# Performance work log

Hardware: AMD Instinct MI355X
Metric: run time of the kernel (lower is better)

Reference implementation:

```python
import jax, jax.numpy as jnp
import numpy as np

MAX_LENGTH = 256
WIDTH = 4


def _attention_matrix(a, b):
    # a, b: (B, M, D) with M = max_length + width - 1
    # euclidean match score: 1 / (1 + ||a_i - b_j||_2)
    sq = (
        jnp.sum(a * a, axis=-1)[:, :, None]
        + jnp.sum(b * b, axis=-1)[:, None, :]
        - 2.0 * jnp.einsum('bid,bjd->bij', a, b)
    )
    dist = jnp.sqrt(jnp.maximum(sq, 0.0))
    return 1.0 / (1.0 + dist)  # (B, M, M)


def reference(x1, x2):
    # x1, x2: (B, 1, M, D), M = MAX_LENGTH + WIDTH - 1
    a = x1[:, 0]  # (B, M, D)
    b = x2[:, 0]
    A = _attention_matrix(a, b)  # (B, M, M), A[b,i,j] = score(a_i, b_j)
    # row_sum over dim i of A[:,:,k] weights x1 column k; col analogously for x2.
    w_a = jnp.sum(A, axis=1)  # (B, M): sum_i A[i, k]
    w_b = jnp.sum(A, axis=2)  # (B, M): sum_j A[k, j]
    y1 = w_a[:, :, None] * a  # (B, M, D)
    y2 = w_b[:, :, None] * b
    # sliding-window sum of width WIDTH: w[j] = sum_{k=j}^{j+WIDTH-1} y[k]
    w1 = sum(y1[:, d:d + MAX_LENGTH, :] for d in range(WIDTH))
    w2 = sum(y2[:, d:d + MAX_LENGTH, :] for d in range(WIDTH))
    return (w1[:, None], w2[:, None])  # (B, 1, MAX_LENGTH, D) each


def setup_inputs() -> dict:
    key = jax.random.key(0)
    k1, k2 = jax.random.split(key)
    B, M, D = 128, MAX_LENGTH + WIDTH - 1, 512
    x1 = jax.random.normal(k1, (B, 1, M, D), dtype=jnp.float32)
    x2 = jax.random.normal(k2, (B, 1, M, D), dtype=jnp.float32)
    return {"x1": x1, "x2": x2}
```

## Files before the change

### kernel.cpp

```cpp
#include <hip/hip_runtime.h>

#define BATCH 128
#define M 259
#define D 512
#define T 256
#define NM (BATCH * M)
#define OUTHALF (BATCH * T * D)

typedef __bf16 bf16;
typedef __bf16 bf16x4 __attribute__((ext_vector_type(4)));
typedef __bf16 bf16x8 __attribute__((ext_vector_type(8)));
typedef float f32x4 __attribute__((ext_vector_type(4)));


__global__ void k_norms(const float* __restrict__ x1, const float* __restrict__ x2,
                        float* __restrict__ ws) {
    int wave = blockIdx.x * 4 + (threadIdx.x >> 6);
    int lane = threadIdx.x & 63;
    if (wave >= NM) return;
    const float4* p1 = (const float4*)(x1 + (size_t)wave * D);
    const float4* p2 = (const float4*)(x2 + (size_t)wave * D);
    float s1 = 0.f, s2 = 0.f;
#pragma unroll
    for (int q = 0; q < 2; ++q) {
        float4 v = p1[lane + q * 64];
        s1 += v.x * v.x + v.y * v.y + v.z * v.z + v.w * v.w;
        float4 w = p2[lane + q * 64];
        s2 += w.x * w.x + w.y * w.y + w.z * w.z + w.w * w.w;
    }
#pragma unroll
    for (int off = 32; off > 0; off >>= 1) {
        s1 += __shfl_xor(s1, off);
        s2 += __shfl_xor(s2, off);
    }
    if (lane == 0) {
        ws[wave]          = s1;
        ws[NM + wave]     = s2;
        ws[2 * NM + wave] = 0.f;
        ws[3 * NM + wave] = 0.f;
    }
}

#define BT 96
#define BK 64
#define NTL 3

__launch_bounds__(256)
__global__ void k_pairs(const float* __restrict__ x1, const float* __restrict__ x2,
                        float* __restrict__ ws) {
    __shared__ __align__(16) bf16 As[BT * BK];
    __shared__ __align__(16) bf16 Bs[BT * BK];

    int s   = blockIdx.x;
    int bid = (s & 7) * 144 + (s >> 3);
    int b   = bid / 9;
    int ti  = (bid % 9) / 3;
    int tj  = bid % 3;
    int i0  = ti * BT, j0 = tj * BT;

    int t    = threadIdx.x;
    int lane = t & 63;
    int w    = t >> 6;
    int wm   = w >> 1, wn = w & 1;
    int iw   = i0 + wm * 48;
    int jw   = j0 + wn * 48;

    const float* Ab = x1 + (size_t)b * M * D;
    const float* Bb = x2 + (size_t)b * M * D;

    const float* pa[6];
    const float* pb[6];
    int c4 = (t & 15) * 4;
#pragma unroll
    for (int p = 0; p < 6; ++p) {
        int ra = min(i0 + p * 16 + (t >> 4), M - 1);
        int rb = min(j0 + p * 16 + (t >> 4), M - 1);
        pa[p] = Ab + (size_t)ra * D + c4;
        pb[p] = Bb + (size_t)rb * D + c4;
    }
    int wslot   = (t & 15) >> 1;
    int wwithin = (t & 1) * 4;
    int wr_off[6];
#pragma unroll
    for (int p = 0; p < 6; ++p) {
        int row = p * 16 + (t >> 4);
        wr_off[p] = row * BK + ((wslot ^ (row & 7)) << 3) + wwithin;
    }

    int a_off[3][2], b_off[3][2];
#pragma unroll
    for (int fm = 0; fm < 3; ++fm) {
        int rowa = wm * 48 + fm * 16 + (lane & 15);
        int rowb = wn * 48 + fm * 16 + (lane & 15);
#pragma unroll
        for (int kk = 0; kk < 2; ++kk) {
            int slot = kk * 4 + (lane >> 4);
            a_off[fm][kk] = rowa * BK + ((slot ^ (rowa & 7)) << 3);
            b_off[fm][kk] = rowb * BK + ((slot ^ (rowb & 7)) << 3);
        }
    }

    f32x4 acc[3][3];
#pragma unroll
    for (int fm = 0; fm < 3; ++fm)
#pragma unroll
        for (int fn = 0; fn < 3; ++fn) acc[fm][fn] = (f32x4)0.f;

    for (int k0 = 0; k0 < D; k0 += BK) {
        float4 va[6], vb[6];
#pragma unroll
        for (int p = 0; p < 6; ++p) {
            va[p] = *(const float4*)(pa[p] + k0);
            vb[p] = *(const float4*)(pb[p] + k0);
        }
        __syncthreads();
#pragma unroll
        for (int p = 0; p < 6; ++p) {
            bf16x4 ca = { (bf16)va[p].x, (bf16)va[p].y, (bf16)va[p].z, (bf16)va[p].w };
            bf16x4 cb = { (bf16)vb[p].x, (bf16)vb[p].y, (bf16)vb[p].z, (bf16)vb[p].w };
            *(bf16x4*)&As[wr_off[p]] = ca;
            *(bf16x4*)&Bs[wr_off[p]] = cb;
        }
        __syncthreads();
#pragma unroll
        for (int kk = 0; kk < 2; ++kk) {
            bf16x8 af[3], bfr[3];
#pragma unroll
            for (int fm = 0; fm < 3; ++fm) af[fm]  = *(const bf16x8*)&As[a_off[fm][kk]];
#pragma unroll
            for (int fn = 0; fn < 3; ++fn) bfr[fn] = *(const bf16x8*)&Bs[b_off[fn][kk]];
#pragma unroll
            for (int fm = 0; fm < 3; ++fm)
#pragma unroll
                for (int fn = 0; fn < 3; ++fn)
                    acc[fm][fn] = __builtin_amdgcn_mfma_f32_16x16x32_bf16(
                        af[fm], bfr[fn], acc[fm][fn], 0, 0, 0);
        }
    }

    int b_off_w = b * M;
    float na_[3][4], nb_[3];
#pragma unroll
    for (int fm = 0; fm < 3; ++fm)
#pragma unroll
        for (int r = 0; r < 4; ++r) {
            int i = iw + fm * 16 + (lane >> 4) * 4 + r;
            na_[fm][r] = (i < M) ? ws[b_off_w + i] : 0.f;
        }
#pragma unroll
    for (int fn = 0; fn < 3; ++fn) {
        int j = jw + fn * 16 + (lane & 15);
        nb_[fn] = (j < M) ? ws[NM + b_off_w + j] : 0.f;
    }

    float rs[3][4];
    float cs[3];
#pragma unroll
    for (int fm = 0; fm < 3; ++fm)
#pragma unroll
        for (int r = 0; r < 4; ++r) rs[fm][r] = 0.f;
#pragma unroll
    for (int fn = 0; fn < 3; ++fn) cs[fn] = 0.f;

#pragma unroll
    for (int fm = 0; fm < 3; ++fm) {
#pragma unroll
        for (int fn = 0; fn < 3; ++fn) {
#pragma unroll
            for (int r = 0; r < 4; ++r) {
                int i = iw + fm * 16 + (lane >> 4) * 4 + r;
                int j = jw + fn * 16 + (lane & 15);
                float av = 0.f;
                if (i < M && j < M) {
                    float sq   = na_[fm][r] + nb_[fn] - 2.f * acc[fm][fn][r];
                    float dist = sqrtf(fmaxf(sq, 0.f));
                    av = 1.f / (1.f + dist);
                }
                rs[fm][r] += av;
                cs[fn]    += av;
            }
        }
    }

#pragma unroll
    for (int fm = 0; fm < 3; ++fm)
#pragma unroll
        for (int r = 0; r < 4; ++r) {
            float v = rs[fm][r];
            v += __shfl_xor(v, 1); v += __shfl_xor(v, 2);
            v += __shfl_xor(v, 4); v += __shfl_xor(v, 8);
            int i = iw + fm * 16 + (lane >> 4) * 4 + r;
            if ((lane & 15) == 0 && i < M) atomicAdd(&ws[3 * NM + b_off_w + i], v);
        }
#pragma unroll
    for (int fn = 0; fn < 3; ++fn) {
        float v = cs[fn];
        v += __shfl_xor(v, 16); v += __shfl_xor(v, 32);
        int j = jw + fn * 16 + (lane & 15);
        if ((lane >> 4) == 0 && j < M) atomicAdd(&ws[2 * NM + b_off_w + j], v);
    }
}

__global__ void k_out(const float* __restrict__ x1, const float* __restrict__ x2,
                      const float* __restrict__ ws, float* __restrict__ out) {
    int bid   = blockIdx.x;
    int which = bid & 1;
    int dh    = (bid >> 1) & 1;
    int tc    = (bid >> 2) & 3;
    int b     = bid >> 4;
    int d     = dh * 256 + threadIdx.x;
    const float* src  = which ? x2 : x1;
    const float* w    = ws + (which ? 3 * NM : 2 * NM) + b * M;
    const float* rows = src + (size_t)b * M * D + d;
    float* o = out + (size_t)which * OUTHALF + ((size_t)b * T + tc * 64) * D + d;
    int t0 = tc * 64;
    float v0 = rows[(size_t)(t0 + 0) * D];
    float v1 = rows[(size_t)(t0 + 1) * D];
    float v2 = rows[(size_t)(t0 + 2) * D];
    float s0 = w[t0 + 0], s1 = w[t0 + 1], s2 = w[t0 + 2];
    for (int tt = 0; tt < 64; ++tt) {
        int tg = t0 + tt;
        float v3 = rows[(size_t)(tg + 3) * D];
        float s3 = w[tg + 3];
        o[(size_t)tt * D] = s0 * v0 + s1 * v1 + s2 * v2 + s3 * v3;
        v0 = v1; v1 = v2; v2 = v3;
        s0 = s1; s1 = s2; s2 = s3;
    }
}

extern "C" void kernel_launch(void* const* d_in, const int* in_sizes, int n_in,
                              void* d_out, int out_size, void* d_ws, size_t ws_size,
                              hipStream_t stream) {
    const float* x1 = (const float*)d_in[0];
    const float* x2 = (const float*)d_in[1];
    float* out = (float*)d_out;
    float* ws  = (float*)d_ws;

    k_norms<<<NM / 4, 256, 0, stream>>>(x1, x2, ws);
    k_pairs<<<BATCH * NTL * NTL, 256, 0, stream>>>(x1, x2, ws);
    k_out<<<BATCH * 16, 256, 0, stream>>>(x1, x2, ws, out);
}
```

Baseline: 112.6 us.

## Fuse row norms into pair GEMM, prefetch next K tile, vectorize output kernel

Drops the separate norm kernel: squared norms are now accumulated from the fp32 tiles already loaded in the pairwise GEMM and shared through LDS, which removes a full extra read of both inputs. A small zeroing kernel replaces it for the atomic accumulators. The GEMM loop also software-prefetches the next K slice into registers before the MMA work. The output kernel switches to float4 loads and stores with 32-row chunks and 128 threads. Costs are higher register pressure in k_pairs, and each tile now recomputes the norms of rows it shares with other tiles.

New measurement: 125.3 us. 11.3% more time.

```diff
diff --git a/kernel.cpp b/kernel.cpp
--- a/kernel.cpp
+++ b/kernel.cpp
@@ -13,32 +13,9 @@
 typedef float f32x4 __attribute__((ext_vector_type(4)));
 
 
-__global__ void k_norms(const float* __restrict__ x1, const float* __restrict__ x2,
-                        float* __restrict__ ws) {
-    int wave = blockIdx.x * 4 + (threadIdx.x >> 6);
-    int lane = threadIdx.x & 63;
-    if (wave >= NM) return;
-    const float4* p1 = (const float4*)(x1 + (size_t)wave * D);
-    const float4* p2 = (const float4*)(x2 + (size_t)wave * D);
-    float s1 = 0.f, s2 = 0.f;
-#pragma unroll
-    for (int q = 0; q < 2; ++q) {
-        float4 v = p1[lane + q * 64];
-        s1 += v.x * v.x + v.y * v.y + v.z * v.z + v.w * v.w;
-        float4 w = p2[lane + q * 64];
-        s2 += w.x * w.x + w.y * w.y + w.z * w.z + w.w * w.w;
-    }
-#pragma unroll
-    for (int off = 32; off > 0; off >>= 1) {
-        s1 += __shfl_xor(s1, off);
-        s2 += __shfl_xor(s2, off);
-    }
-    if (lane == 0) {
-        ws[wave]          = s1;
-        ws[NM + wave]     = s2;
-        ws[2 * NM + wave] = 0.f;
-        ws[3 * NM + wave] = 0.f;
-    }
+__global__ void k_zero(float4* __restrict__ ws4) {
+    int i = blockIdx.x * 256 + threadIdx.x;
+    if (i < (2 * NM + 3) / 4) ws4[i] = make_float4(0.f, 0.f, 0.f, 0.f);
 }
 
 #define BT 96
@@ -50,6 +27,8 @@
                         float* __restrict__ ws) {
     __shared__ __align__(16) bf16 As[BT * BK];
     __shared__ __align__(16) bf16 Bs[BT * BK];
+    __shared__ float na_s[BT];
+    __shared__ float nb_s[BT];
 
     int s   = blockIdx.x;
     int bid = (s & 7) * 144 + (s >> 3);
@@ -106,20 +85,40 @@
 #pragma unroll
         for (int fn = 0; fn < 3; ++fn) acc[fm][fn] = (f32x4)0.f;
 
+    float sa[6], sb[6];
+#pragma unroll
+    for (int p = 0; p < 6; ++p) { sa[p] = 0.f; sb[p] = 0.f; }
+
+    float4 va[6], vb[6];
+#pragma unroll
+    for (int p = 0; p < 6; ++p) {
+        va[p] = *(const float4*)(pa[p]);
+        vb[p] = *(const float4*)(pb[p]);
+    }
+
     for (int k0 = 0; k0 < D; k0 += BK) {
-        float4 va[6], vb[6];
+        bf16x4 ca[6], cb[6];
 #pragma unroll
         for (int p = 0; p < 6; ++p) {
-            va[p] = *(const float4*)(pa[p] + k0);
-            vb[p] = *(const float4*)(pb[p] + k0);
+            sa[p] += va[p].x * va[p].x + va[p].y * va[p].y
+                   + va[p].z * va[p].z + va[p].w * va[p].w;
+            sb[p] += vb[p].x * vb[p].x + vb[p].y * vb[p].y
+                   + vb[p].z * vb[p].z + vb[p].w * vb[p].w;
+            ca[p] = { (bf16)va[p].x, (bf16)va[p].y, (bf16)va[p].z, (bf16)va[p].w };
+            cb[p] = { (bf16)vb[p].x, (bf16)vb[p].y, (bf16)vb[p].z, (bf16)vb[p].w };
         }
         __syncthreads();
 #pragma unroll
         for (int p = 0; p < 6; ++p) {
-            bf16x4 ca = { (bf16)va[p].x, (bf16)va[p].y, (bf16)va[p].z, (bf16)va[p].w };
-            bf16x4 cb = { (bf16)vb[p].x, (bf16)vb[p].y, (bf16)vb[p].z, (bf16)vb[p].w };
-            *(bf16x4*)&As[wr_off[p]] = ca;
-            *(bf16x4*)&Bs[wr_off[p]] = cb;
+            *(bf16x4*)&As[wr_off[p]] = ca[p];
+            *(bf16x4*)&Bs[wr_off[p]] = cb[p];
+        }
+        if (k0 + BK < D) {
+#pragma unroll
+            for (int p = 0; p < 6; ++p) {
+                va[p] = *(const float4*)(pa[p] + k0 + BK);
+                vb[p] = *(const float4*)(pb[p] + k0 + BK);
+            }
         }
         __syncthreads();
 #pragma unroll
@@ -138,20 +137,30 @@
         }
     }
 
+#pragma unroll
+    for (int p = 0; p < 6; ++p) {
+        float v1 = sa[p], v2 = sb[p];
+        v1 += __shfl_xor(v1, 1); v1 += __shfl_xor(v1, 2);
+        v1 += __shfl_xor(v1, 4); v1 += __shfl_xor(v1, 8);
+        v2 += __shfl_xor(v2, 1); v2 += __shfl_xor(v2, 2);
+        v2 += __shfl_xor(v2, 4); v2 += __shfl_xor(v2, 8);
+        if ((t & 15) == 0) {
+            na_s[p * 16 + (t >> 4)] = v1;
+            nb_s[p * 16 + (t >> 4)] = v2;
+        }
+    }
+    __syncthreads();
+
     int b_off_w = b * M;
     float na_[3][4], nb_[3];
 #pragma unroll
     for (int fm = 0; fm < 3; ++fm)
 #pragma unroll
-        for (int r = 0; r < 4; ++r) {
-            int i = iw + fm * 16 + (lane >> 4) * 4 + r;
-            na_[fm][r] = (i < M) ? ws[b_off_w + i] : 0.f;
-        }
-#pragma unroll
-    for (int fn = 0; fn < 3; ++fn) {
-        int j = jw + fn * 16 + (lane & 15);
-        nb_[fn] = (j < M) ? ws[NM + b_off_w + j] : 0.f;
-    }
+        for (int r = 0; r < 4; ++r)
+            na_[fm][r] = na_s[wm * 48 + fm * 16 + (lane >> 4) * 4 + r];
+#pragma unroll
+    for (int fn = 0; fn < 3; ++fn)
+        nb_[fn] = nb_s[wn * 48 + fn * 16 + (lane & 15)];
 
     float rs[3][4];
     float cs[3];
@@ -190,14 +199,14 @@
             v += __shfl_xor(v, 1); v += __shfl_xor(v, 2);
             v += __shfl_xor(v, 4); v += __shfl_xor(v, 8);
             int i = iw + fm * 16 + (lane >> 4) * 4 + r;
-            if ((lane & 15) == 0 && i < M) atomicAdd(&ws[3 * NM + b_off_w + i], v);
+            if ((lane & 15) == 0 && i < M) atomicAdd(&ws[NM + b_off_w + i], v);
         }
 #pragma unroll
     for (int fn = 0; fn < 3; ++fn) {
         float v = cs[fn];
         v += __shfl_xor(v, 16); v += __shfl_xor(v, 32);
         int j = jw + fn * 16 + (lane & 15);
-        if ((lane >> 4) == 0 && j < M) atomicAdd(&ws[2 * NM + b_off_w + j], v);
+        if ((lane >> 4) == 0 && j < M) atomicAdd(&ws[b_off_w + j], v);
     }
 }
 
@@ -205,24 +214,28 @@
                       const float* __restrict__ ws, float* __restrict__ out) {
     int bid   = blockIdx.x;
     int which = bid & 1;
-    int dh    = (bid >> 1) & 1;
-    int tc    = (bid >> 2) & 3;
+    int tc    = (bid >> 1) & 7;
     int b     = bid >> 4;
-    int d     = dh * 256 + threadIdx.x;
+    int d4    = threadIdx.x << 2;
     const float* src  = which ? x2 : x1;
-    const float* w    = ws + (which ? 3 * NM : 2 * NM) + b * M;
-    const float* rows = src + (size_t)b * M * D + d;
-    float* o = out + (size_t)which * OUTHALF + ((size_t)b * T + tc * 64) * D + d;
-    int t0 = tc * 64;
-    float v0 = rows[(size_t)(t0 + 0) * D];
-    float v1 = rows[(size_t)(t0 + 1) * D];
-    float v2 = rows[(size_t)(t0 + 2) * D];
-    float s0 = w[t0 + 0], s1 = w[t0 + 1], s2 = w[t0 + 2];
-    for (int tt = 0; tt < 64; ++tt) {
-        int tg = t0 + tt;
-        float v3 = rows[(size_t)(tg + 3) * D];
-        float s3 = w[tg + 3];
-        o[(size_t)tt * D] = s0 * v0 + s1 * v1 + s2 * v2 + s3 * v3;
+    const float* wgt  = ws + (which ? NM : 0) + b * M;
+    const float* rows = src + (size_t)b * M * D + d4;
+    float* o = out + (size_t)which * OUTHALF + ((size_t)b * T + tc * 32) * D + d4;
+    int t0 = tc * 32;
+    float4 v0 = *(const float4*)(rows + (size_t)(t0 + 0) * D);
+    float4 v1 = *(const float4*)(rows + (size_t)(t0 + 1) * D);
+    float4 v2 = *(const float4*)(rows + (size_t)(t0 + 2) * D);
+    float s0 = wgt[t0 + 0], s1 = wgt[t0 + 1], s2 = wgt[t0 + 2];
+#pragma unroll 4
+    for (int tt = 0; tt < 32; ++tt) {
+        float4 v3 = *(const float4*)(rows + (size_t)(t0 + tt + 3) * D);
+        float s3  = wgt[t0 + tt + 3];
+        float4 r;
+        r.x = s0 * v0.x + s1 * v1.x + s2 * v2.x + s3 * v3.x;
+        r.y = s0 * v0.y + s1 * v1.y + s2 * v2.y + s3 * v3.y;
+        r.z = s0 * v0.z + s1 * v1.z + s2 * v2.z + s3 * v3.z;
+        r.w = s0 * v0.w + s1 * v1.w + s2 * v2.w + s3 * v3.w;
+        *(float4*)(o + (size_t)tt * D) = r;
         v0 = v1; v1 = v2; v2 = v3;
         s0 = s1; s1 = s2; s2 = s3;
     }
@@ -236,7 +249,7 @@
     float* out = (float*)d_out;
     float* ws  = (float*)d_ws;
 
-    k_norms<<<NM / 4, 256, 0, stream>>>(x1, x2, ws);
+    k_zero<<<(2 * NM / 4 + 255) / 256, 256, 0, stream>>>((float4*)ws);
     k_pairs<<<BATCH * NTL * NTL, 256, 0, stream>>>(x1, x2, ws);
-    k_out<<<BATCH * 16, 256, 0, stream>>>(x1, x2, ws, out);
-}
+    k_out<<<BATCH * 16, 128, 0, stream>>>(x1, x2, ws, out);
+}
```

## Double-buffer LDS tiles in pair GEMM and vectorize sliding-window output kernel

Applied to the files above, without the earlier changes.

The pair kernel now uses two LDS buffers, so the bf16 conversion and store of the next K tile and the global prefetch of the tile after it are issued after the MFMAs on the current tile. This cuts the two barriers per K step down to one and hides global load latency behind compute, at the cost of doubled LDS use (about 49KB per block), which could lower occupancy. The output kernel switches to float4 loads and stores with 128 threads, each block covering 32 rows, to cut the instruction count of this memory-bound pass.

Result: slower. 117.3 us (+4.2%).

```diff
diff --git a/kernel.cpp b/kernel.cpp
--- a/kernel.cpp
+++ b/kernel.cpp
@@ -48,8 +48,8 @@
 __launch_bounds__(256)
 __global__ void k_pairs(const float* __restrict__ x1, const float* __restrict__ x2,
                         float* __restrict__ ws) {
-    __shared__ __align__(16) bf16 As[BT * BK];
-    __shared__ __align__(16) bf16 Bs[BT * BK];
+    __shared__ __align__(16) bf16 As[2][BT * BK];
+    __shared__ __align__(16) bf16 Bs[2][BT * BK];
 
     int s   = blockIdx.x;
     int bid = (s & 7) * 144 + (s >> 3);
@@ -106,35 +106,58 @@
 #pragma unroll
         for (int fn = 0; fn < 3; ++fn) acc[fm][fn] = (f32x4)0.f;
 
+    float4 va[6], vb[6];
+#pragma unroll
+    for (int p = 0; p < 6; ++p) {
+        va[p] = *(const float4*)(pa[p]);
+        vb[p] = *(const float4*)(pb[p]);
+    }
+#pragma unroll
+    for (int p = 0; p < 6; ++p) {
+        bf16x4 ca = { (bf16)va[p].x, (bf16)va[p].y, (bf16)va[p].z, (bf16)va[p].w };
+        bf16x4 cb = { (bf16)vb[p].x, (bf16)vb[p].y, (bf16)vb[p].z, (bf16)vb[p].w };
+        *(bf16x4*)&As[0][wr_off[p]] = ca;
+        *(bf16x4*)&Bs[0][wr_off[p]] = cb;
+    }
+    __syncthreads();
+#pragma unroll
+    for (int p = 0; p < 6; ++p) {
+        va[p] = *(const float4*)(pa[p] + BK);
+        vb[p] = *(const float4*)(pb[p] + BK);
+    }
+
     for (int k0 = 0; k0 < D; k0 += BK) {
-        float4 va[6], vb[6];
-#pragma unroll
-        for (int p = 0; p < 6; ++p) {
-            va[p] = *(const float4*)(pa[p] + k0);
-            vb[p] = *(const float4*)(pb[p] + k0);
-        }
-        __syncthreads();
-#pragma unroll
-        for (int p = 0; p < 6; ++p) {
-            bf16x4 ca = { (bf16)va[p].x, (bf16)va[p].y, (bf16)va[p].z, (bf16)va[p].w };
-            bf16x4 cb = { (bf16)vb[p].x, (bf16)vb[p].y, (bf16)vb[p].z, (bf16)vb[p].w };
-            *(bf16x4*)&As[wr_off[p]] = ca;
-            *(bf16x4*)&Bs[wr_off[p]] = cb;
-        }
-        __syncthreads();
+        int cur = (k0 >> 6) & 1;
 #pragma unroll
         for (int kk = 0; kk < 2; ++kk) {
             bf16x8 af[3], bfr[3];
 #pragma unroll
-            for (int fm = 0; fm < 3; ++fm) af[fm]  = *(const bf16x8*)&As[a_off[fm][kk]];
-#pragma unroll
-            for (int fn = 0; fn < 3; ++fn) bfr[fn] = *(const bf16x8*)&Bs[b_off[fn][kk]];
+            for (int fm = 0; fm < 3; ++fm) af[fm]  = *(const bf16x8*)&As[cur][a_off[fm][kk]];
+#pragma unroll
+            for (int fn = 0; fn < 3; ++fn) bfr[fn] = *(const bf16x8*)&Bs[cur][b_off[fn][kk]];
 #pragma unroll
             for (int fm = 0; fm < 3; ++fm)
 #pragma unroll
                 for (int fn = 0; fn < 3; ++fn)
                     acc[fm][fn] = __builtin_amdgcn_mfma_f32_16x16x32_bf16(
                         af[fm], bfr[fn], acc[fm][fn], 0, 0, 0);
+        }
+        if (k0 + BK < D) {
+#pragma unroll
+            for (int p = 0; p < 6; ++p) {
+                bf16x4 ca = { (bf16)va[p].x, (bf16)va[p].y, (bf16)va[p].z, (bf16)va[p].w };
+                bf16x4 cb = { (bf16)vb[p].x, (bf16)vb[p].y, (bf16)vb[p].z, (bf16)vb[p].w };
+                *(bf16x4*)&As[cur ^ 1][wr_off[p]] = ca;
+                *(bf16x4*)&Bs[cur ^ 1][wr_off[p]] = cb;
+            }
+            __syncthreads();
+            if (k0 + 2 * BK < D) {
+#pragma unroll
+                for (int p = 0; p < 6; ++p) {
+                    va[p] = *(const float4*)(pa[p] + k0 + 2 * BK);
+                    vb[p] = *(const float4*)(pb[p] + k0 + 2 * BK);
+                }
+            }
         }
     }
 
@@ -205,24 +228,28 @@
                       const float* __restrict__ ws, float* __restrict__ out) {
     int bid   = blockIdx.x;
     int which = bid & 1;
-    int dh    = (bid >> 1) & 1;
-    int tc    = (bid >> 2) & 3;
+    int tc    = (bid >> 1) & 7;
     int b     = bid >> 4;
-    int d     = dh * 256 + threadIdx.x;
+    int d4    = threadIdx.x << 2;
     const float* src  = which ? x2 : x1;
-    const float* w    = ws + (which ? 3 * NM : 2 * NM) + b * M;
-    const float* rows = src + (size_t)b * M * D + d;
-    float* o = out + (size_t)which * OUTHALF + ((size_t)b * T + tc * 64) * D + d;
-    int t0 = tc * 64;
-    float v0 = rows[(size_t)(t0 + 0) * D];
-    float v1 = rows[(size_t)(t0 + 1) * D];
-    float v2 = rows[(size_t)(t0 + 2) * D];
-    float s0 = w[t0 + 0], s1 = w[t0 + 1], s2 = w[t0 + 2];
-    for (int tt = 0; tt < 64; ++tt) {
-        int tg = t0 + tt;
-        float v3 = rows[(size_t)(tg + 3) * D];
-        float s3 = w[tg + 3];
-        o[(size_t)tt * D] = s0 * v0 + s1 * v1 + s2 * v2 + s3 * v3;
+    const float* wgt  = ws + (which ? 3 * NM : 2 * NM) + b * M;
+    const float* rows = src + (size_t)b * M * D + d4;
+    float* o = out + (size_t)which * OUTHALF + ((size_t)b * T + tc * 32) * D + d4;
+    int t0 = tc * 32;
+    float4 v0 = *(const float4*)(rows + (size_t)(t0 + 0) * D);
+    float4 v1 = *(const float4*)(rows + (size_t)(t0 + 1) * D);
+    float4 v2 = *(const float4*)(rows + (size_t)(t0 + 2) * D);
+    float s0 = wgt[t0 + 0], s1 = wgt[t0 + 1], s2 = wgt[t0 + 2];
+#pragma unroll 4
+    for (int tt = 0; tt < 32; ++tt) {
+        float4 v3 = *(const float4*)(rows + (size_t)(t0 + tt + 3) * D);
+        float s3  = wgt[t0 + tt + 3];
+        float4 r;
+        r.x = s0 * v0.x + s1 * v1.x + s2 * v2.x + s3 * v3.x;
+        r.y = s0 * v0.y + s1 * v1.y + s2 * v2.y + s3 * v3.y;
+        r.z = s0 * v0.z + s1 * v1.z + s2 * v2.z + s3 * v3.z;
+        r.w = s0 * v0.w + s1 * v1.w + s2 * v2.w + s3 * v3.w;
+        *(float4*)(o + (size_t)tt * D) = r;
         v0 = v1; v1 = v2; v2 = v3;
         s0 = s1; s1 = s2; s2 = s3;
     }
@@ -238,5 +265,5 @@
 
     k_norms<<<NM / 4, 256, 0, stream>>>(x1, x2, ws);
     k_pairs<<<BATCH * NTL * NTL, 256, 0, stream>>>(x1, x2, ws);
-    k_out<<<BATCH * 16, 256, 0, stream>>>(x1, x2, ws, out);
-}
+    k_out<<<BATCH * 16, 128, 0, stream>>>(x1, x2, ws, out);
+}
```
